# Kernel tuning notes

Hardware: AMD Instinct MI355X
Metric: run time of the kernel (lower is better)

Reference implementation:

```python
import jax, jax.numpy as jnp
import numpy as np

STRIDES = [4, 8, 16, 32]
OUT = 7                 # output_size
CANON_SIZE = 224.0      # canonical_box_size
CANON_LVL = 4           # canonical_level
MIN_LVL, MAX_LVL = 2, 5 # log2 of min/max stride
ALIGNED = False


def setup_inputs() -> dict:
    key = jax.random.key(0)
    ks = jax.random.split(key, 6)
    N, C, L, IMG = 2, 256, 256, 1024
    inp = {}
    for i, s in enumerate(STRIDES):
        inp['feat%d' % i] = jax.random.normal(ks[i], (N, C, IMG // s, IMG // s), dtype=jnp.float32)
    # boxes in image coords, sizes 16..512 px so the FPN level assignment spans P2..P5
    cxy = jax.random.uniform(ks[4], (N, L, 2), dtype=jnp.float32) * IMG
    wh = jax.random.uniform(ks[5], (N, L, 2), dtype=jnp.float32) * 496.0 + 16.0
    x1y1 = jnp.clip(cxy - wh / 2, 0.0, IMG - 1.0)
    x2y2 = jnp.clip(cxy + wh / 2, 0.0, IMG - 1.0)
    inp['boxes'] = jnp.concatenate([x1y1, x2y2], axis=-1)  # [N, L, 4] (x1,y1,x2,y2)
    return inp


def _roi_align_level(feat, boxes, bidx, scale):
    # feat [N,C,H,W]; boxes [R,4] image coords; sampling_ratio=1, bilinear
    N, C, H, W = feat.shape
    offset = 0.5 if ALIGNED else 0.0
    x1 = boxes[:, 0] * scale - offset
    y1 = boxes[:, 1] * scale - offset
    x2 = boxes[:, 2] * scale - offset
    y2 = boxes[:, 3] * scale - offset
    roi_w, roi_h = x2 - x1, y2 - y1
    if not ALIGNED:  # legacy behavior: force rois to be at least 1x1
        roi_w = jnp.maximum(roi_w, 1.0)
        roi_h = jnp.maximum(roi_h, 1.0)
    bin_h = roi_h / OUT
    bin_w = roi_w / OUT
    grid = jnp.arange(OUT, dtype=jnp.float32) + 0.5
    ys = y1[:, None] + grid * bin_h[:, None]  # [R, OUT] one sample per bin (ratio=1)
    xs = x1[:, None] + grid * bin_w[:, None]
    vy = (ys > -1.0) & (ys < H)
    vx = (xs > -1.0) & (xs < W)
    y = jnp.clip(ys, 0.0, H - 1.0)
    x = jnp.clip(xs, 0.0, W - 1.0)
    y0 = jnp.clip(jnp.floor(y), 0, H - 2).astype(jnp.int32)
    x0 = jnp.clip(jnp.floor(x), 0, W - 2).astype(jnp.int32)
    ly = y - y0
    lx = x - x0
    ft = jnp.transpose(feat, (0, 2, 3, 1))  # [N,H,W,C] for channel-contiguous gathers
    b = bidx[:, None, None]
    yi = y0[:, :, None]
    xi = x0[:, None, :]
    v00 = ft[b, yi, xi]        # [R,OUT,OUT,C]
    v01 = ft[b, yi, xi + 1]
    v10 = ft[b, yi + 1, xi]
    v11 = ft[b, yi + 1, xi + 1]
    wy1 = ly[:, :, None, None]
    wx1 = lx[:, None, :, None]
    wy0 = 1.0 - wy1
    wx0 = 1.0 - wx1
    val = wy0 * wx0 * v00 + wy0 * wx1 * v01 + wy1 * wx0 * v10 + wy1 * wx1 * v11
    mask = (vy[:, :, None] & vx[:, None, :])[..., None]
    val = jnp.where(mask, val, 0.0)
    return jnp.transpose(val, (0, 3, 1, 2))  # [R,C,OUT,OUT]


def reference(feat0, feat1, feat2, feat3, boxes):
    feats = [feat0, feat1, feat2, feat3]
    N, L, _ = boxes.shape
    R = N * L
    bxs = boxes.reshape(R, 4)
    bidx = jnp.repeat(jnp.arange(N), L)
    # detectron-style level assignment from box area in image coords
    area = jnp.maximum(bxs[:, 2] - bxs[:, 0], 0.0) * jnp.maximum(bxs[:, 3] - bxs[:, 1], 0.0)
    lvl = jnp.floor(CANON_LVL + jnp.log2(jnp.sqrt(area) / CANON_SIZE + 1e-8))
    lvl = jnp.clip(lvl, MIN_LVL, MAX_LVL).astype(jnp.int32) - MIN_LVL  # [R] in 0..3
    outs = jnp.stack([_roi_align_level(f, bxs, bidx, 1.0 / s) for f, s in zip(feats, STRIDES)])
    out = outs[lvl, jnp.arange(R)]  # select assigned level per box -> [R,C,OUT,OUT]
    return out
```

## Files before the change

kernel.cpp:

```cpp
#include <hip/hip_runtime.h>
#include <hip/hip_bf16.h>


#define C_DIM 256
#define OUTB 7
#define NBINS 49
#define PER_ROI 12544
#define NROI 512
#define CPB 8
#define OUTS_PB (CPB * NBINS)
#define TPB 256
#define NXCD 8

__global__ __launch_bounds__(TPB) void msroi_xcd_kernel(
    const float* __restrict__ f0, const float* __restrict__ f1,
    const float* __restrict__ f2, const float* __restrict__ f3,
    const float* __restrict__ boxes, float* __restrict__ out) {
  const int d      = blockIdx.x;
  const int xcd    = d & (NXCD - 1);
  const int s      = d >> 3;
  const int r      = s >> 2;
  const int cgroup = xcd * 4 + (s & 3);
  const int cb     = cgroup * CPB;
  const int n      = r >> 8;
  const int tid    = threadIdx.x;

  const float4 box = ((const float4*)boxes)[r];

  float bwp = fmaxf(box.z - box.x, 0.0f);
  float bhp = fmaxf(box.w - box.y, 0.0f);
  float lv = floorf(4.0f + log2f(sqrtf(bwp * bhp) / 224.0f + 1e-8f));
  const int lvl = (int)(fminf(fmaxf(lv, 2.0f), 5.0f)) - 2;

  const float* __restrict__ feat;
  switch (lvl) {
    case 0:  feat = f0; break;
    case 1:  feat = f1; break;
    case 2:  feat = f2; break;
    default: feat = f3; break;
  }
  const int sh = 8 - lvl;
  const int H = 1 << sh, W = H;
  const int hw_sh = 2 * sh;
  const float scale = 1.0f / (float)(4 << lvl);

  const float x1 = box.x * scale, y1 = box.y * scale;
  const float x2 = box.z * scale, y2 = box.w * scale;
  const float roi_w = fmaxf(x2 - x1, 1.0f);
  const float roi_h = fmaxf(y2 - y1, 1.0f);
  const float bin_w = roi_w / (float)OUTB;
  const float bin_h = roi_h / (float)OUTB;

  float* __restrict__ obase = out + (size_t)r * PER_ROI + (size_t)cb * NBINS;

#pragma unroll
  for (int half = 0; half < 2; half++) {
    const int le = tid + half * TPB;
    if (le >= OUTS_PB) break;
    const int cl  = le / NBINS;
    const int bin = le - cl * NBINS;
    const int py  = bin / OUTB;
    const int px  = bin - py * OUTB;

    const float ysf = __fadd_rn(y1, __fmul_rn((float)py + 0.5f, bin_h));
    const float xsf = __fadd_rn(x1, __fmul_rn((float)px + 0.5f, bin_w));
    const bool vy = (ysf > -1.0f) && (ysf < (float)H);
    const bool vx = (xsf > -1.0f) && (xsf < (float)W);
    const float vm = (vy && vx) ? 1.0f : 0.0f;

    float y = fminf(fmaxf(ysf, 0.0f), (float)(H - 1));
    float x = fminf(fmaxf(xsf, 0.0f), (float)(W - 1));
    const int y0 = min((int)floorf(y), H - 2);
    const int x0 = min((int)floorf(x), W - 2);
    const float ly = y - (float)y0;
    const float lx = x - (float)x0;
    const float wy0 = 1.0f - ly, wx0 = 1.0f - lx;

    const float* __restrict__ p =
        feat + (((size_t)(n * C_DIM + cb + cl)) << hw_sh) +
        ((size_t)y0 << sh) + (size_t)x0;
    const float2 v0 = *reinterpret_cast<const float2*>(p);
    const float2 v1 = *reinterpret_cast<const float2*>(p + W);

    const float val =
        vm * (wy0 * (wx0 * v0.x + lx * v0.y) + ly * (wx0 * v1.x + lx * v1.y));
    __builtin_nontemporal_store(val, obase + le);
  }
}

extern "C" void kernel_launch(void* const* d_in, const int* in_sizes, int n_in,
                              void* d_out, int out_size, void* d_ws, size_t ws_size,
                              hipStream_t stream) {
  const float* f0 = (const float*)d_in[0];
  const float* f1 = (const float*)d_in[1];
  const float* f2 = (const float*)d_in[2];
  const float* f3 = (const float*)d_in[3];
  const float* boxes = (const float*)d_in[4];
  float* out = (float*)d_out;

  dim3 grid(NROI * (C_DIM / CPB));
  dim3 block(TPB);
  msroi_xcd_kernel<<<grid, block, 0, stream>>>(f0, f1, f2, f3, boxes, out);
}
```

Measured before the change: 26.59 us.

## Sort ROIs by pyramid level and widen channel blocks per workgroup

Adds a single-block pre-kernel that computes each box's FPN level and writes a level-sorted permutation into workspace. The main kernel now visits ROIs in that order and gives each block 32 channels instead of 8, looping over outputs with a stride. Grouping same-level ROIs aims for better cache locality on the feature maps, and wider blocks amortize per-block box setup across more channels. The cost is an extra serial kernel launch with O(N) loops per thread, plus fewer, longer blocks.

```diff
diff --git a/kernel.cpp b/kernel.cpp
--- a/kernel.cpp
+++ b/kernel.cpp
@@ -7,29 +7,57 @@
 #define NBINS 49
 #define PER_ROI 12544
 #define NROI 512
-#define CPB 8
+#define CPB 32
 #define OUTS_PB (CPB * NBINS)
 #define TPB 256
 #define NXCD 8
 
+__global__ __launch_bounds__(NROI) void lvlsort_k(
+    const float* __restrict__ boxes, int* __restrict__ perm) {
+  __shared__ int lvl_of[NROI];
+  __shared__ int base[4];
+  const int t = threadIdx.x;
+  const float4 b = ((const float4*)boxes)[t];
+  const float bw = fmaxf(b.z - b.x, 0.0f);
+  const float bh = fmaxf(b.w - b.y, 0.0f);
+  const float lv = floorf(4.0f + log2f(sqrtf(bw * bh) / 224.0f + 1e-8f));
+  const int l = (int)(fminf(fmaxf(lv, 2.0f), 5.0f)) - 2;
+  lvl_of[t] = l;
+  __syncthreads();
+  if (t < 4) {
+    int c = 0;
+    for (int i = 0; i < NROI; i++) c += (lvl_of[i] == t);
+    base[t] = c;
+  }
+  __syncthreads();
+  if (t == 0) {
+    int s = 0;
+    for (int k = 0; k < 4; k++) { int c = base[k]; base[k] = s; s += c; }
+  }
+  __syncthreads();
+  int rank = 0;
+  for (int i = 0; i < t; i++) rank += (lvl_of[i] == l);
+  perm[base[l] + rank] = t;
+}
+
 __global__ __launch_bounds__(TPB) void msroi_xcd_kernel(
     const float* __restrict__ f0, const float* __restrict__ f1,
     const float* __restrict__ f2, const float* __restrict__ f3,
-    const float* __restrict__ boxes, float* __restrict__ out) {
-  const int d      = blockIdx.x;
-  const int xcd    = d & (NXCD - 1);
-  const int s      = d >> 3;
-  const int r      = s >> 2;
-  const int cgroup = xcd * 4 + (s & 3);
-  const int cb     = cgroup * CPB;
-  const int n      = r >> 8;
-  const int tid    = threadIdx.x;
+    const float* __restrict__ boxes, const int* __restrict__ perm,
+    float* __restrict__ out) {
+  const int d   = blockIdx.x;
+  const int xcd = d & (NXCD - 1);
+  const int s   = d >> 3;
+  const int r   = perm[s];
+  const int cb  = xcd * CPB;
+  const int n   = r >> 8;
+  const int tid = threadIdx.x;
 
   const float4 box = ((const float4*)boxes)[r];
 
-  float bwp = fmaxf(box.z - box.x, 0.0f);
-  float bhp = fmaxf(box.w - box.y, 0.0f);
-  float lv = floorf(4.0f + log2f(sqrtf(bwp * bhp) / 224.0f + 1e-8f));
+  const float bwp = fmaxf(box.z - box.x, 0.0f);
+  const float bhp = fmaxf(box.w - box.y, 0.0f);
+  const float lv = floorf(4.0f + log2f(sqrtf(bwp * bhp) / 224.0f + 1e-8f));
   const int lvl = (int)(fminf(fmaxf(lv, 2.0f), 5.0f)) - 2;
 
   const float* __restrict__ feat;
@@ -52,11 +80,10 @@
   const float bin_h = roi_h / (float)OUTB;
 
   float* __restrict__ obase = out + (size_t)r * PER_ROI + (size_t)cb * NBINS;
+  const float* __restrict__ fbase =
+      feat + (((size_t)(n * C_DIM + cb)) << hw_sh);
 
-#pragma unroll
-  for (int half = 0; half < 2; half++) {
-    const int le = tid + half * TPB;
-    if (le >= OUTS_PB) break;
+  for (int le = tid; le < OUTS_PB; le += TPB) {
     const int cl  = le / NBINS;
     const int bin = le - cl * NBINS;
     const int py  = bin / OUTB;
@@ -77,8 +104,7 @@
     const float wy0 = 1.0f - ly, wx0 = 1.0f - lx;
 
     const float* __restrict__ p =
-        feat + (((size_t)(n * C_DIM + cb + cl)) << hw_sh) +
-        ((size_t)y0 << sh) + (size_t)x0;
+        fbase + ((size_t)cl << hw_sh) + ((size_t)y0 << sh) + (size_t)x0;
     const float2 v0 = *reinterpret_cast<const float2*>(p);
     const float2 v1 = *reinterpret_cast<const float2*>(p + W);
 
@@ -97,8 +123,9 @@
   const float* f3 = (const float*)d_in[3];
   const float* boxes = (const float*)d_in[4];
   float* out = (float*)d_out;
+  int* perm = (int*)d_ws;
 
-  dim3 grid(NROI * (C_DIM / CPB));
-  dim3 block(TPB);
-  msroi_xcd_kernel<<<grid, block, 0, stream>>>(f0, f1, f2, f3, boxes, out);
+  lvlsort_k<<<1, NROI, 0, stream>>>(boxes, perm);
+  dim3 grid(NROI * NXCD);
+  msroi_xcd_kernel<<<grid, TPB, 0, stream>>>(f0, f1, f2, f3, boxes, perm, out);
 }
```

After: 37.64 us. 1.42x slower.

## Sort ROIs by FPN level so concurrent blocks share feature maps

Applied to the files above, without the earlier changes.

Adds a small single-block pre-kernel that computes each box's FPN level and writes a stable permutation grouping ROIs by level, using wave ballots and a shared-memory prefix. The main kernel then maps block index to ROI through this permutation, so blocks running at the same time read the same feature level and should get better cache locality on gathers. The cost is an extra kernel launch with a serialized dependency, plus one indirect load per block.

```diff
diff --git a/kernel.cpp b/kernel.cpp
--- a/kernel.cpp
+++ b/kernel.cpp
@@ -12,14 +12,47 @@
 #define TPB 256
 #define NXCD 8
 
+__global__ __launch_bounds__(NROI) void lvlsort_k(
+    const float* __restrict__ boxes, int* __restrict__ perm) {
+  const int t = threadIdx.x;
+  const int wave = t >> 6, lane = t & 63;
+  const float4 b = ((const float4*)boxes)[t];
+  const float bw = fmaxf(b.z - b.x, 0.0f);
+  const float bh = fmaxf(b.w - b.y, 0.0f);
+  const float lv = floorf(4.0f + log2f(sqrtf(bw * bh) / 224.0f + 1e-8f));
+  const int l = (int)(fminf(fmaxf(lv, 2.0f), 5.0f)) - 2;
+
+  __shared__ int wcnt[4][8];
+  __shared__ int wbase[4][8];
+  unsigned long long m[4];
+#pragma unroll
+  for (int k = 0; k < 4; k++) {
+    m[k] = __ballot(l == k);
+    if (lane == 0) wcnt[k][wave] = __popcll(m[k]);
+  }
+  __syncthreads();
+  if (t == 0) {
+    int s = 0;
+#pragma unroll
+    for (int k = 0; k < 4; k++)
+#pragma unroll
+      for (int w = 0; w < 8; w++) { wbase[k][w] = s; s += wcnt[k][w]; }
+  }
+  __syncthreads();
+  const unsigned long long below = (lane == 0) ? 0ull : (~0ull >> (64 - lane));
+  const int rank = __popcll(m[l] & below);
+  perm[wbase[l][wave] + rank] = t;
+}
+
 __global__ __launch_bounds__(TPB) void msroi_xcd_kernel(
     const float* __restrict__ f0, const float* __restrict__ f1,
     const float* __restrict__ f2, const float* __restrict__ f3,
-    const float* __restrict__ boxes, float* __restrict__ out) {
+    const float* __restrict__ boxes, const int* __restrict__ perm,
+    float* __restrict__ out) {
   const int d      = blockIdx.x;
   const int xcd    = d & (NXCD - 1);
   const int s      = d >> 3;
-  const int r      = s >> 2;
+  const int r      = perm[s >> 2];
   const int cgroup = xcd * 4 + (s & 3);
   const int cb     = cgroup * CPB;
   const int n      = r >> 8;
@@ -27,9 +60,9 @@
 
   const float4 box = ((const float4*)boxes)[r];
 
-  float bwp = fmaxf(box.z - box.x, 0.0f);
-  float bhp = fmaxf(box.w - box.y, 0.0f);
-  float lv = floorf(4.0f + log2f(sqrtf(bwp * bhp) / 224.0f + 1e-8f));
+  const float bwp = fmaxf(box.z - box.x, 0.0f);
+  const float bhp = fmaxf(box.w - box.y, 0.0f);
+  const float lv = floorf(4.0f + log2f(sqrtf(bwp * bhp) / 224.0f + 1e-8f));
   const int lvl = (int)(fminf(fmaxf(lv, 2.0f), 5.0f)) - 2;
 
   const float* __restrict__ feat;
@@ -97,8 +130,9 @@
   const float* f3 = (const float*)d_in[3];
   const float* boxes = (const float*)d_in[4];
   float* out = (float*)d_out;
+  int* perm = (int*)d_ws;
 
+  lvlsort_k<<<1, NROI, 0, stream>>>(boxes, perm);
   dim3 grid(NROI * (C_DIM / CPB));
-  dim3 block(TPB);
-  msroi_xcd_kernel<<<grid, block, 0, stream>>>(f0, f1, f2, f3, boxes, out);
+  msroi_xcd_kernel<<<grid, TPB, 0, stream>>>(f0, f1, f2, f3, boxes, perm, out);
 }
```

New measurement: 33.46 us. 1.26x slower.
